# Kernel tuning notes

Measured on AMD Instinct MI355X. Metric: run time of the kernel, lower is better.

The kernel has to match this reference:

```python
import jax, jax.numpy as jnp
import numpy as np

B, G, N, C = 8, 16, 1024, 256


def setup_inputs() -> dict:
    key = jax.random.key(0)
    k1, k2, k3, k4, k5 = jax.random.split(key, 5)
    x = jax.random.normal(k1, (B, G, N, C), dtype=jnp.float32)
    vs = jax.random.normal(k2, (B, G, 1, N, 3), dtype=jnp.float32)
    s = 1.0 / np.sqrt(C)
    W_fc = jax.random.normal(k3, (C, C), dtype=jnp.float32) * s   # nn.Linear weight [out,in]
    b_fc = jax.random.normal(k4, (C,), dtype=jnp.float32) * s
    W_vn = jax.random.normal(k5, (C, C), dtype=jnp.float32) * s   # VNLinear weight [out,in], no bias
    return {"x": x, "vs": vs, "W_fc": W_fc, "b_fc": b_fc, "W_vn": W_vn}


def reference(x, vs, W_fc, b_fc, W_vn):
    # q = fc(x): [B,G,N,C]
    q = jnp.einsum('bgnc,oc->bgno', x, W_fc) + b_fc
    # softmax over the point dim N (torch dim=2)
    atten = jax.nn.softmax(q, axis=2)
    xw = atten * x  # [B,G,N,C]
    # torch: expand to [B,G,C,N,3] * vs then sum over N.
    # Equivalent contraction without materializing the 5D tensor:
    v = jnp.squeeze(vs, axis=2)  # [B,G,N,3]
    out = jnp.einsum('bgnc,bgnd->bgcd', xw, v)  # [B,G,C,3]
    # VNLinear: bias-free linear over channel dim, shared across the 3 vector comps
    return jnp.einsum('bgcd,oc->bgod', out, W_vn)  # [B,G,C,3]
```

## Files before the change

### kernel.cpp

```cpp
#include <hip/hip_runtime.h>
#include <hip/hip_bf16.h>


#define NQ 1024
#define CQ 256
#define RT 32
#define TILES 8
#define WB_OFF 131072

typedef __attribute__((ext_vector_type(8))) short bf16x8;
typedef __attribute__((ext_vector_type(4))) float f32x4;

__device__ __forceinline__ ushort2 pk2(float a, float b) {
    __hip_bfloat162 h = __float22bfloat162_rn(make_float2(a, b));
    ushort2 r;
    __builtin_memcpy(&r, &h, sizeof(r));
    return r;
}
__device__ __forceinline__ float bf2f(ushort h) {
    union { unsigned u; float f; } v; v.u = ((unsigned)h) << 16;
    return v.f;
}

__device__ __forceinline__ void gload16(const float* g, float* l) {
    __builtin_amdgcn_global_load_lds(
        (const __attribute__((address_space(1))) unsigned int*)g,
        (__attribute__((address_space(3))) unsigned int*)l, 16, 0, 0);
}

__device__ __forceinline__ void bar_lgkm() {
    __builtin_amdgcn_sched_barrier(0);
    asm volatile("s_waitcnt lgkmcnt(0)" ::: "memory");
    __builtin_amdgcn_sched_barrier(0);
    __builtin_amdgcn_s_barrier();
    __builtin_amdgcn_sched_barrier(0);
}

__global__ __launch_bounds__(256)
void wfc_cvt(const float* __restrict__ Wfc, ushort* __restrict__ WbT) {
    const int i = blockIdx.x * 256 + threadIdx.x;
    const int o = i >> 6;
    const int k4 = (i & 63) * 4;
    float4 v = *reinterpret_cast<const float4*>(Wfc + (size_t)o * CQ + k4);
    ushort2 a0 = pk2(v.x, v.y), a1 = pk2(v.z, v.w);
    ushort4 pk = { a0.x, a0.y, a1.x, a1.y };
    *reinterpret_cast<ushort4*>(WbT + ((size_t)(k4 >> 3) * CQ + o) * 8 + (k4 & 7)) = pk;
}

__global__ __launch_bounds__(512, 2)
void attn_pool_partial(const float* __restrict__ x, const float* __restrict__ vs,
                       const ushort* __restrict__ WbT, float* __restrict__ ws) {
    __shared__ __align__(16) float land[RT * CQ];
    __shared__ __align__(16) char  bx[2][RT * 512];
    __shared__ __align__(16) float vsm[TILES * RT * 3];

    const int t = threadIdx.x;
    const int id = blockIdx.x;
    const int bg = id >> 2;
    const int ntg = id & 3;
    const int nb = ntg * (TILES * RT);

    const int w = t >> 6, lane = t & 63;
    const int quad = lane >> 4, l16 = lane & 15;

    const float* xb = x + (size_t)bg * NQ * CQ;
    const float* vb = vs + (size_t)bg * NQ * 3;

    bf16x8 Bf0[8], Bf1[8];
    const int bcol0 = w * 32 + l16;
    #pragma unroll
    for (int ks = 0; ks < 8; ++ks) {
        const size_t fo = (size_t)(ks * 4 + quad) * (CQ * 8);
        Bf0[ks] = *reinterpret_cast<const bf16x8*>(WbT + fo + (size_t)bcol0 * 8);
        Bf1[ks] = *reinterpret_cast<const bf16x8*>(WbT + fo + (size_t)(bcol0 + 16) * 8);
    }
    __builtin_amdgcn_sched_barrier(0);

    const bool vload = (t < 192);
    float4 vreg;
    if (vload) vreg = reinterpret_cast<const float4*>(vb + (size_t)nb * 3)[t];
    __builtin_amdgcn_sched_barrier(0);

    #pragma unroll
    for (int p = 0; p < 4; ++p) {
        const int row = p * 8 + w;
        gload16(xb + (size_t)(nb + row) * CQ + lane * 4, &land[row * CQ]);
    }
    __builtin_amdgcn_sched_barrier(0);
    asm volatile("s_waitcnt vmcnt(0)" ::: "memory");
    __builtin_amdgcn_sched_barrier(0);
    if (vload) reinterpret_cast<float4*>(vsm)[t] = vreg;
    bar_lgkm();

    {
        char* dst = bx[0];
        #pragma unroll
        for (int p = 0; p < 4; ++p) {
            const int row = p * 8 + w;
            float4 v4 = *reinterpret_cast<const float4*>(&land[row * CQ + lane * 4]);
            ushort2 a0 = pk2(v4.x, v4.y), a1 = pk2(v4.z, v4.w);
            ushort4 pk = { a0.x, a0.y, a1.x, a1.y };
            *reinterpret_cast<ushort4*>(dst + row * 512 + ((lane * 8) ^ ((row & 7) << 4))) = pk;
        }
    }
    bar_lgkm();

    float rZ[2] = {0.f, 0.f}, rS0[2] = {0.f, 0.f}, rS1[2] = {0.f, 0.f}, rS2[2] = {0.f, 0.f};

    for (int i = 0; i < TILES; ++i) {
        const char* bxp = bx[i & 1];

        if (i < TILES - 1) {
            const int tb = nb + (i + 1) * RT;
            #pragma unroll
            for (int p = 0; p < 4; ++p) {
                const int row = p * 8 + w;
                gload16(xb + (size_t)(tb + row) * CQ + lane * 4, &land[row * CQ]);
            }
        }
        __builtin_amdgcn_sched_barrier(0);

        f32x4 acc[2][2];
        #pragma unroll
        for (int mi = 0; mi < 2; ++mi)
            #pragma unroll
            for (int ci = 0; ci < 2; ++ci) acc[mi][ci] = (f32x4){0.f, 0.f, 0.f, 0.f};

        __builtin_amdgcn_s_setprio(1);
        #pragma unroll
        for (int ks = 0; ks < 8; ++ks) {
            const int kkb = ks * 64 + quad * 16;
            #pragma unroll
            for (int mi = 0; mi < 2; ++mi) {
                const int row = mi * 16 + l16;
                bf16x8 a = *reinterpret_cast<const bf16x8*>(
                    bxp + row * 512 + (kkb ^ ((row & 7) << 4)));
                acc[mi][0] = __builtin_amdgcn_mfma_f32_16x16x32_bf16(a, Bf0[ks], acc[mi][0], 0, 0, 0);
                acc[mi][1] = __builtin_amdgcn_mfma_f32_16x16x32_bf16(a, Bf1[ks], acc[mi][1], 0, 0, 0);
            }
        }
        __builtin_amdgcn_s_setprio(0);

        const float* vt = vsm + (size_t)(i * RT) * 3;
        #pragma unroll
        for (int mi = 0; mi < 2; ++mi) {
            const int rbase = mi * 16 + quad * 4;
            float v0[4], v1[4], v2[4];
            #pragma unroll
            for (int r = 0; r < 4; ++r) {
                v0[r] = vt[(rbase + r) * 3 + 0];
                v1[r] = vt[(rbase + r) * 3 + 1];
                v2[r] = vt[(rbase + r) * 3 + 2];
            }
            #pragma unroll
            for (int ci = 0; ci < 2; ++ci) {
                const int xc = w * 32 + ci * 16 + l16;
                #pragma unroll
                for (int r = 0; r < 4; ++r) {
                    const int row = rbase + r;
                    float e = __expf(acc[mi][ci][r]);
                    ushort h = *reinterpret_cast<const ushort*>(
                        bxp + row * 512 + ((xc * 2) ^ ((row & 7) << 4)));
                    float xv = bf2f(h);
                    rZ[ci] += e;
                    float p = e * xv;
                    rS0[ci] = fmaf(p, v0[r], rS0[ci]);
                    rS1[ci] = fmaf(p, v1[r], rS1[ci]);
                    rS2[ci] = fmaf(p, v2[r], rS2[ci]);
                }
            }
        }

        __builtin_amdgcn_sched_barrier(0);
        asm volatile("s_waitcnt vmcnt(0)" ::: "memory");
        __builtin_amdgcn_sched_barrier(0);
        __builtin_amdgcn_s_barrier();
        __builtin_amdgcn_sched_barrier(0);

        if (i < TILES - 1) {
            char* dst = bx[(i + 1) & 1];
            #pragma unroll
            for (int p = 0; p < 4; ++p) {
                const int row = p * 8 + w;
                float4 v4 = *reinterpret_cast<const float4*>(&land[row * CQ + lane * 4]);
                ushort2 a0 = pk2(v4.x, v4.y), a1 = pk2(v4.z, v4.w);
                ushort4 pk = { a0.x, a0.y, a1.x, a1.y };
                *reinterpret_cast<ushort4*>(dst + row * 512 + ((lane * 8) ^ ((row & 7) << 4))) = pk;
            }
            bar_lgkm();
        }
    }

    #pragma unroll
    for (int ci = 0; ci < 2; ++ci) {
        float z = rZ[ci], s0 = rS0[ci], s1 = rS1[ci], s2 = rS2[ci];
        #pragma unroll
        for (int off = 16; off < 64; off <<= 1) {
            z  += __shfl_xor(z,  off);
            s0 += __shfl_xor(s0, off);
            s1 += __shfl_xor(s1, off);
            s2 += __shfl_xor(s2, off);
        }
        if (quad == 0) {
            const int col = w * 32 + ci * 16 + l16;
            float* p = ws + ((size_t)bg * CQ + col) * 4;
            atomicAdd(&p[0], z);
            atomicAdd(&p[1], s0);
            atomicAdd(&p[2], s1);
            atomicAdd(&p[3], s2);
        }
    }
}

__global__ __launch_bounds__(256, 4)
void vn_linear(const float* __restrict__ ws, const float* __restrict__ Wvn,
               float* __restrict__ out) {
    __shared__ float Tsm[CQ][3];
    const int bg = blockIdx.x, t = threadIdx.x;
    {
        f32x4 z4 = *reinterpret_cast<const f32x4*>(ws + ((size_t)bg * CQ + t) * 4);
        float inv = 1.f / z4[0];
        Tsm[t][0] = z4[1] * inv;
        Tsm[t][1] = z4[2] * inv;
        Tsm[t][2] = z4[3] * inv;
    }
    __syncthreads();
    const float* wr = Wvn + (size_t)t * CQ;
    float a0 = 0.f, a1 = 0.f, a2 = 0.f;
    #pragma unroll
    for (int c = 0; c < CQ; c += 4) {
        float4 w4 = *reinterpret_cast<const float4*>(wr + c);
        a0 += w4.x * Tsm[c + 0][0] + w4.y * Tsm[c + 1][0]
            + w4.z * Tsm[c + 2][0] + w4.w * Tsm[c + 3][0];
        a1 += w4.x * Tsm[c + 0][1] + w4.y * Tsm[c + 1][1]
            + w4.z * Tsm[c + 2][1] + w4.w * Tsm[c + 3][1];
        a2 += w4.x * Tsm[c + 0][2] + w4.y * Tsm[c + 1][2]
            + w4.z * Tsm[c + 2][2] + w4.w * Tsm[c + 3][2];
    }
    float* op = out + ((size_t)bg * CQ + t) * 3;
    op[0] = a0; op[1] = a1; op[2] = a2;
}

extern "C" void kernel_launch(void* const* d_in, const int* in_sizes, int n_in,
                              void* d_out, int out_size, void* d_ws, size_t ws_size,
                              hipStream_t stream) {
    const float* x   = (const float*)d_in[0];
    const float* vs  = (const float*)d_in[1];
    const float* Wfc = (const float*)d_in[2];
    const float* Wvn = (const float*)d_in[4];
    float* out = (float*)d_out;
    float* ws  = (float*)d_ws;

    ushort* WbT = (ushort*)(ws + WB_OFF);

    (void)hipMemsetAsync(ws, 0, (size_t)128 * CQ * 4 * sizeof(float), stream);
    wfc_cvt<<<dim3(64), dim3(256), 0, stream>>>(Wfc, WbT);
    attn_pool_partial<<<dim3(512), dim3(512), 0, stream>>>(x, vs, WbT, ws);
    vn_linear<<<dim3(128), dim3(256), 0, stream>>>(ws, Wvn, out);
}
```

Measured before the change: 216.7 us.

## Halve block to 4 waves, each computing 64 output columns with more register weights

```diff
diff --git a/kernel.cpp b/kernel.cpp
--- a/kernel.cpp
+++ b/kernel.cpp
@@ -47,12 +47,12 @@
     *reinterpret_cast<ushort4*>(WbT + ((size_t)(k4 >> 3) * CQ + o) * 8 + (k4 & 7)) = pk;
 }
 
-__global__ __launch_bounds__(512, 2)
+__global__ __launch_bounds__(256, 2)
 void attn_pool_partial(const float* __restrict__ x, const float* __restrict__ vs,
                        const ushort* __restrict__ WbT, float* __restrict__ ws) {
     __shared__ __align__(16) float land[RT * CQ];
     __shared__ __align__(16) char  bx[2][RT * 512];
-    __shared__ __align__(16) float vsm[TILES * RT * 3];
+    __shared__ __align__(16) float vsmP[3][TILES * RT];
 
     const int t = threadIdx.x;
     const int id = blockIdx.x;
@@ -66,13 +66,16 @@
     const float* xb = x + (size_t)bg * NQ * CQ;
     const float* vb = vs + (size_t)bg * NQ * 3;
 
-    bf16x8 Bf0[8], Bf1[8];
-    const int bcol0 = w * 32 + l16;
-    #pragma unroll
-    for (int ks = 0; ks < 8; ++ks) {
-        const size_t fo = (size_t)(ks * 4 + quad) * (CQ * 8);
-        Bf0[ks] = *reinterpret_cast<const bf16x8*>(WbT + fo + (size_t)bcol0 * 8);
-        Bf1[ks] = *reinterpret_cast<const bf16x8*>(WbT + fo + (size_t)(bcol0 + 16) * 8);
+    bf16x8 Bf[4][8];
+    const int bcol0 = w * 64 + l16;
+    #pragma unroll
+    for (int ci = 0; ci < 4; ++ci) {
+        #pragma unroll
+        for (int ks = 0; ks < 8; ++ks) {
+            const size_t fo = (size_t)(ks * 4 + quad) * (CQ * 8);
+            Bf[ci][ks] = *reinterpret_cast<const bf16x8*>(
+                WbT + fo + (size_t)(bcol0 + ci * 16) * 8);
+        }
     }
     __builtin_amdgcn_sched_barrier(0);
 
@@ -82,21 +85,28 @@
     __builtin_amdgcn_sched_barrier(0);
 
     #pragma unroll
-    for (int p = 0; p < 4; ++p) {
-        const int row = p * 8 + w;
+    for (int p = 0; p < 8; ++p) {
+        const int row = p * 4 + w;
         gload16(xb + (size_t)(nb + row) * CQ + lane * 4, &land[row * CQ]);
     }
     __builtin_amdgcn_sched_barrier(0);
     asm volatile("s_waitcnt vmcnt(0)" ::: "memory");
     __builtin_amdgcn_sched_barrier(0);
-    if (vload) reinterpret_cast<float4*>(vsm)[t] = vreg;
+    if (vload) {
+        float va[4] = { vreg.x, vreg.y, vreg.z, vreg.w };
+        #pragma unroll
+        for (int j = 0; j < 4; ++j) {
+            const int e = t * 4 + j;
+            vsmP[e % 3][e / 3] = va[j];
+        }
+    }
     bar_lgkm();
 
     {
         char* dst = bx[0];
         #pragma unroll
-        for (int p = 0; p < 4; ++p) {
-            const int row = p * 8 + w;
+        for (int p = 0; p < 8; ++p) {
+            const int row = p * 4 + w;
             float4 v4 = *reinterpret_cast<const float4*>(&land[row * CQ + lane * 4]);
             ushort2 a0 = pk2(v4.x, v4.y), a1 = pk2(v4.z, v4.w);
             ushort4 pk = { a0.x, a0.y, a1.x, a1.y };
@@ -105,7 +115,10 @@
     }
     bar_lgkm();
 
-    float rZ[2] = {0.f, 0.f}, rS0[2] = {0.f, 0.f}, rS1[2] = {0.f, 0.f}, rS2[2] = {0.f, 0.f};
+    float rZ[4] = {0.f, 0.f, 0.f, 0.f};
+    float rS0[4] = {0.f, 0.f, 0.f, 0.f};
+    float rS1[4] = {0.f, 0.f, 0.f, 0.f};
+    float rS2[4] = {0.f, 0.f, 0.f, 0.f};
 
     for (int i = 0; i < TILES; ++i) {
         const char* bxp = bx[i & 1];
@@ -113,18 +126,18 @@
         if (i < TILES - 1) {
             const int tb = nb + (i + 1) * RT;
             #pragma unroll
-            for (int p = 0; p < 4; ++p) {
-                const int row = p * 8 + w;
+            for (int p = 0; p < 8; ++p) {
+                const int row = p * 4 + w;
                 gload16(xb + (size_t)(tb + row) * CQ + lane * 4, &land[row * CQ]);
             }
         }
         __builtin_amdgcn_sched_barrier(0);
 
-        f32x4 acc[2][2];
+        f32x4 acc[2][4];
         #pragma unroll
         for (int mi = 0; mi < 2; ++mi)
             #pragma unroll
-            for (int ci = 0; ci < 2; ++ci) acc[mi][ci] = (f32x4){0.f, 0.f, 0.f, 0.f};
+            for (int ci = 0; ci < 4; ++ci) acc[mi][ci] = (f32x4){0.f, 0.f, 0.f, 0.f};
 
         __builtin_amdgcn_s_setprio(1);
         #pragma unroll
@@ -135,26 +148,23 @@
                 const int row = mi * 16 + l16;
                 bf16x8 a = *reinterpret_cast<const bf16x8*>(
                     bxp + row * 512 + (kkb ^ ((row & 7) << 4)));
-                acc[mi][0] = __builtin_amdgcn_mfma_f32_16x16x32_bf16(a, Bf0[ks], acc[mi][0], 0, 0, 0);
-                acc[mi][1] = __builtin_amdgcn_mfma_f32_16x16x32_bf16(a, Bf1[ks], acc[mi][1], 0, 0, 0);
+                #pragma unroll
+                for (int ci = 0; ci < 4; ++ci)
+                    acc[mi][ci] = __builtin_amdgcn_mfma_f32_16x16x32_bf16(a, Bf[ci][ks], acc[mi][ci], 0, 0, 0);
             }
         }
         __builtin_amdgcn_s_setprio(0);
 
-        const float* vt = vsm + (size_t)(i * RT) * 3;
         #pragma unroll
         for (int mi = 0; mi < 2; ++mi) {
             const int rbase = mi * 16 + quad * 4;
-            float v0[4], v1[4], v2[4];
-            #pragma unroll
-            for (int r = 0; r < 4; ++r) {
-                v0[r] = vt[(rbase + r) * 3 + 0];
-                v1[r] = vt[(rbase + r) * 3 + 1];
-                v2[r] = vt[(rbase + r) * 3 + 2];
-            }
-            #pragma unroll
-            for (int ci = 0; ci < 2; ++ci) {
-                const int xc = w * 32 + ci * 16 + l16;
+            const int vrow = i * RT + rbase;
+            f32x4 v0 = *reinterpret_cast<const f32x4*>(&vsmP[0][vrow]);
+            f32x4 v1 = *reinterpret_cast<const f32x4*>(&vsmP[1][vrow]);
+            f32x4 v2 = *reinterpret_cast<const f32x4*>(&vsmP[2][vrow]);
+            #pragma unroll
+            for (int ci = 0; ci < 4; ++ci) {
+                const int xc = w * 64 + ci * 16 + l16;
                 #pragma unroll
                 for (int r = 0; r < 4; ++r) {
                     const int row = rbase + r;
@@ -180,8 +190,8 @@
         if (i < TILES - 1) {
             char* dst = bx[(i + 1) & 1];
             #pragma unroll
-            for (int p = 0; p < 4; ++p) {
-                const int row = p * 8 + w;
+            for (int p = 0; p < 8; ++p) {
+                const int row = p * 4 + w;
                 float4 v4 = *reinterpret_cast<const float4*>(&land[row * CQ + lane * 4]);
                 ushort2 a0 = pk2(v4.x, v4.y), a1 = pk2(v4.z, v4.w);
                 ushort4 pk = { a0.x, a0.y, a1.x, a1.y };
@@ -192,7 +202,7 @@
     }
 
     #pragma unroll
-    for (int ci = 0; ci < 2; ++ci) {
+    for (int ci = 0; ci < 4; ++ci) {
         float z = rZ[ci], s0 = rS0[ci], s1 = rS1[ci], s2 = rS2[ci];
         #pragma unroll
         for (int off = 16; off < 64; off <<= 1) {
@@ -202,7 +212,7 @@
             s2 += __shfl_xor(s2, off);
         }
         if (quad == 0) {
-            const int col = w * 32 + ci * 16 + l16;
+            const int col = w * 64 + ci * 16 + l16;
             float* p = ws + ((size_t)bg * CQ + col) * 4;
             atomicAdd(&p[0], z);
             atomicAdd(&p[1], s0);
@@ -255,6 +265,6 @@
 
     (void)hipMemsetAsync(ws, 0, (size_t)128 * CQ * 4 * sizeof(float), stream);
     wfc_cvt<<<dim3(64), dim3(256), 0, stream>>>(Wfc, WbT);
-    attn_pool_partial<<<dim3(512), dim3(512), 0, stream>>>(x, vs, WbT, ws);
+    attn_pool_partial<<<dim3(512), dim3(256), 0, stream>>>(x, vs, WbT, ws);
     vn_linear<<<dim3(128), dim3(256), 0, stream>>>(ws, Wvn, out);
 }
```

Result: slower. 309.7 us (+42.9%).
